# Performance work log

Hardware: AMD Instinct MI355X
Metric: run time of the kernel (lower is better)

Reference implementation:

```python
import jax, jax.numpy as jnp
import numpy as np
import math

D_MODEL = 1024
N_HEADS = 16
D_HEAD = D_MODEL // N_HEADS


def layer_norm(x, gamma, beta, eps=1e-5):
    mu = jnp.mean(x, axis=-1, keepdims=True)
    var = jnp.var(x, axis=-1, keepdims=True)
    return (x - mu) / jnp.sqrt(var + eps) * gamma + beta


def setup_inputs() -> dict:
    key = jax.random.key(0)
    ks = jax.random.split(key, 12)
    B, T, d = 4, 2048, D_MODEL
    s = 0.02
    x = jax.random.normal(ks[0], (B, T, d), dtype=jnp.float32)
    t = jnp.arange(B * T, dtype=jnp.float32).reshape(B, T) % T  # continuous positions
    return {
        "x": x,
        "t": t,
        "w_qkv": jax.random.normal(ks[1], (d, 3 * d), dtype=jnp.float32) * s,
        "b_qkv": jnp.zeros((3 * d,), jnp.float32),
        "w_proj": jax.random.normal(ks[2], (d, d), dtype=jnp.float32) * s,
        "b_proj": jnp.zeros((d,), jnp.float32),
        "g1": jnp.ones((d,), jnp.float32),
        "beta1": jnp.zeros((d,), jnp.float32),
        "g2": jnp.ones((d,), jnp.float32),
        "beta2": jnp.zeros((d,), jnp.float32),
        "w_mlp1": jax.random.normal(ks[3], (d, 4 * d), dtype=jnp.float32) * s,
        "b_mlp1": jnp.zeros((4 * d,), jnp.float32),
        "w_mlp2": jax.random.normal(ks[4], (4 * d, d), dtype=jnp.float32) * s,
        "b_mlp2": jnp.zeros((d,), jnp.float32),
    }


def reference(x, t, w_qkv, b_qkv, w_proj, b_proj, g1, beta1, g2, beta2, w_mlp1, b_mlp1, w_mlp2, b_mlp2):
    B, T, d = x.shape
    H, dh = N_HEADS, D_HEAD
    scale = dh ** -0.5

    h = layer_norm(x, g1, beta1)
    qkv = h @ w_qkv + b_qkv  # [B,T,3d]
    q, k, v = jnp.split(qkv, 3, axis=-1)
    # [B,T,H,dh] -> [B,H,T,dh]
    q = q.reshape(B, T, H, dh).transpose(0, 2, 1, 3)
    k = k.reshape(B, T, H, dh).transpose(0, 2, 1, 3)
    v = v.reshape(B, T, H, dh).transpose(0, 2, 1, 3)

    # ContinuousRoPE on d_head
    half = dh // 2
    freqs = jnp.exp(jnp.arange(half, dtype=jnp.float32) * (-math.log(10000.0) / (half - 1)))
    args = t[:, :, None] * freqs  # [B,T,half]
    cos = jnp.tile(jnp.cos(args), (1, 1, 2))[:, None]  # [B,1,T,dh]
    sin = jnp.tile(jnp.sin(args), (1, 1, 2))[:, None]

    def rotate_half(u):
        u1, u2 = u[..., :dh // 2], u[..., dh // 2:]
        return jnp.concatenate((-u2, u1), axis=-1)

    q = q * cos + rotate_half(q) * sin
    k = k * cos + rotate_half(k) * sin

    attn = jnp.einsum("bhqd,bhkd->bhqk", q, k) * scale  # [B,H,T,T]
    causal = jnp.tril(jnp.ones((T, T), dtype=bool))
    attn = jnp.where(causal, attn, -jnp.inf)
    attn = jax.nn.softmax(attn, axis=-1)
    o = jnp.einsum("bhqk,bhkd->bhqd", attn, v)  # [B,H,T,dh]
    o = o.transpose(0, 2, 1, 3).reshape(B, T, d)

    x1 = o @ w_proj + b_proj + x
    h2 = layer_norm(x1, g2, beta2)
    mlp = jax.nn.gelu(h2 @ w_mlp1 + b_mlp1, approximate=False) @ w_mlp2 + b_mlp2
    return x1 + mlp
```

## Files before the change

### kernel.cpp

```cpp
#include <hip/hip_runtime.h>

typedef __bf16  bf16x8 __attribute__((ext_vector_type(8)));
typedef float   f32x4  __attribute__((ext_vector_type(4)));

typedef const __attribute__((address_space(1))) void* gas_p;
typedef __attribute__((address_space(3))) void*       las_p;

__device__ __forceinline__ void glds16(const void* g, void* l) {
  __builtin_amdgcn_global_load_lds((gas_p)g, (las_p)l, 16, 0, 0);
}

__device__ __forceinline__ ushort f2bf(float f) {
  unsigned u = __float_as_uint(f);
  u += 0x7fffu + ((u >> 16) & 1u);
  return (ushort)(u >> 16);
}

__device__ __forceinline__ void barx() {
  asm volatile("" ::: "memory");
  __builtin_amdgcn_s_barrier();
  asm volatile("" ::: "memory");
}
#define WAITVM(N) asm volatile("s_waitcnt vmcnt(" #N ")" ::: "memory")

__global__ __launch_bounds__(256) void castT_k(const float* __restrict__ w,
                                               ushort* __restrict__ wT,
                                               const int Kd, const int Nd) {
  __shared__ float t[32][33];
  const int nb = blockIdx.x * 32, kb = blockIdx.y * 32;
  const int tx = threadIdx.x & 31, ty = threadIdx.x >> 5;
#pragma unroll
  for (int r = 0; r < 32; r += 8)
    t[ty + r][tx] = w[(size_t)(kb + ty + r) * Nd + nb + tx];
  __syncthreads();
#pragma unroll
  for (int r = 0; r < 32; r += 8)
    wT[(size_t)(nb + ty + r) * Kd + kb + tx] = f2bf(t[tx][ty + r]);
}

__global__ __launch_bounds__(256) void ln_k(const float* __restrict__ x,
                                            const float* __restrict__ gam,
                                            const float* __restrict__ bet,
                                            ushort* __restrict__ out) {
  const int row = blockIdx.x, tid = threadIdx.x;
  const float4 v = ((const float4*)(x + (size_t)row * 1024))[tid];
  float s  = v.x + v.y + v.z + v.w;
  float sq = v.x * v.x + v.y * v.y + v.z * v.z + v.w * v.w;
#pragma unroll
  for (int o = 32; o > 0; o >>= 1) { s += __shfl_xor(s, o); sq += __shfl_xor(sq, o); }
  __shared__ float red[8];
  const int wid = tid >> 6, lane = tid & 63;
  if (lane == 0) { red[wid] = s; red[4 + wid] = sq; }
  __syncthreads();
  s  = red[0] + red[1] + red[2] + red[3];
  sq = red[4] + red[5] + red[6] + red[7];
  const float mu   = s * (1.0f / 1024.0f);
  const float var  = sq * (1.0f / 1024.0f) - mu * mu;
  const float rstd = rsqrtf(var + 1e-5f);
  const float4 gv = ((const float4*)gam)[tid];
  const float4 bv = ((const float4*)bet)[tid];
  ushort4 o4;
  o4.x = f2bf((v.x - mu) * rstd * gv.x + bv.x);
  o4.y = f2bf((v.y - mu) * rstd * gv.y + bv.y);
  o4.z = f2bf((v.z - mu) * rstd * gv.z + bv.z);
  o4.w = f2bf((v.w - mu) * rstd * gv.w + bv.w);
  ((ushort4*)(out + (size_t)row * 1024))[tid] = o4;
}

__global__ __launch_bounds__(256) void vtrans_k(const ushort* __restrict__ Vn,
                                                ushort* __restrict__ Vt) {
  const int bh = blockIdx.y, i0 = blockIdx.x * 64, tid = threadIdx.x;
  __shared__ ushort t[64][65];
  const ushort* src = Vn + (size_t)bh * (2048 * 64);
#pragma unroll
  for (int kk = 0; kk < 16; ++kk) {
    const int e = tid + kk * 256, r = e >> 6, c = e & 63;
    t[r][c] = src[(size_t)(i0 + r) * 64 + c];
  }
  __syncthreads();
  ushort* dst = Vt + (size_t)bh * (64 * 2048);
#pragma unroll
  for (int kk = 0; kk < 16; ++kk) {
    const int e = tid + kk * 256, r = e >> 6, c = e & 63;
    dst[(size_t)r * 2048 + i0 + c] = t[c][r];
  }
}

template <int MF, int EPI>
__global__ __launch_bounds__(512, 2) void gemm2_k(
    const ushort* __restrict__ A, const ushort* __restrict__ Bt,
    const int M, const int N, const int K,
    const float* __restrict__ bias,
    const float* __restrict__ resid,
    float* __restrict__ outf,
    ushort* __restrict__ outb,
    ushort* __restrict__ qo, ushort* __restrict__ ko, ushort* __restrict__ vo) {
  constexpr int BM = MF * 32;
  constexpr int GA = MF / 4;
  extern __shared__ ushort lds_u[];
  ushort* aL = lds_u;
  ushort* bL = lds_u + 4 * BM * 32;

  const int tid = threadIdx.x, wid = tid >> 6, lane = tid & 63;
  const int l15 = lane & 15, g = lane >> 4;
  const int wr = wid >> 2, wc = wid & 3;
  const int m0 = blockIdx.y * BM, n0 = blockIdx.x * 256;

  const int srl = lane >> 2;
  const int scb = ((lane & 3) << 4) ^ (((lane >> 3) & 3) << 4);
  const int rk  = ((l15 >> 1) & 3) << 4;
  const size_t Krow = (size_t)K * 2;

  auto stageA = [&](int b, int kh, int t) {
#pragma unroll
    for (int L = 0; L < GA; ++L) {
      const char* src = (const char*)A + (size_t)(m0 + L * 128 + wid * 16 + srl) * Krow
                        + (size_t)t * 128 + kh * 64 + scb;
      glds16(src, (char*)aL + (size_t)((b * 2 + kh) * BM + L * 128 + wid * 16) * 64);
    }
  };
  auto stageB = [&](int b, int kh, int t) {
#pragma unroll
    for (int L = 0; L < 2; ++L) {
      const char* src = (const char*)Bt + (size_t)(n0 + L * 128 + wid * 16 + srl) * Krow
                        + (size_t)t * 128 + kh * 64 + scb;
      glds16(src, (char*)bL + (size_t)((b * 2 + kh) * 256 + L * 128 + wid * 16) * 64);
    }
  };

  bf16x8 af[MF], bfr[4];
  f32x4 acc[MF][4] = {};

  auto loadA = [&](int b, int kh) {
#pragma unroll
    for (int m = 0; m < MF; ++m)
      af[m] = *(const bf16x8*)((const char*)aL +
          (size_t)((b * 2 + kh) * BM + wr * (BM / 2) + m * 16 + l15) * 64 + ((g * 16) ^ rk));
  };
  auto loadB = [&](int b, int kh, int nh) {
#pragma unroll
    for (int n = 0; n < 2; ++n)
      bfr[nh * 2 + n] = *(const bf16x8*)((const char*)bL +
          (size_t)((b * 2 + kh) * 256 + wc * 64 + (nh * 2 + n) * 16 + l15) * 64 + ((g * 16) ^ rk));
  };
  auto mfma8 = [&](int nh) {
    __builtin_amdgcn_s_setprio(1);
#pragma unroll
    for (int m = 0; m < MF; ++m) {
      acc[m][nh * 2]     = __builtin_amdgcn_mfma_f32_16x16x32_bf16(af[m], bfr[nh * 2],     acc[m][nh * 2],     0, 0, 0);
      acc[m][nh * 2 + 1] = __builtin_amdgcn_mfma_f32_16x16x32_bf16(af[m], bfr[nh * 2 + 1], acc[m][nh * 2 + 1], 0, 0, 0);
    }
    __builtin_amdgcn_s_setprio(0);
  };

  stageA(0, 0, 0); stageB(0, 0, 0); stageA(0, 1, 0); stageB(0, 1, 0);
  if constexpr (MF == 8) { WAITVM(4); } else { WAITVM(3); }
  barx();

  const int nk = K >> 6;
  int cur = 0;
  for (int t = 0; t < nk; ++t) {
    const bool pf = (t + 1 < nk);
    const int nb = cur ^ 1;
    loadA(cur, 0); loadB(cur, 0, 0);
    if (pf) stageA(nb, 0, t + 1);
    barx();
    mfma8(0);
    barx();
    loadB(cur, 0, 1);
    if (pf) stageB(nb, 0, t + 1);
    barx();
    mfma8(1);
    if (pf) { if constexpr (MF == 8) { WAITVM(4); } else { WAITVM(3); } }
    else    { WAITVM(0); }
    barx();
    loadA(cur, 1); loadB(cur, 1, 0);
    if (pf) stageA(nb, 1, t + 1);
    barx();
    mfma8(0);
    barx();
    loadB(cur, 1, 1);
    if (pf) stageB(nb, 1, t + 1);
    barx();
    mfma8(1);
    if (pf) { if constexpr (MF == 8) { WAITVM(4); } else { WAITVM(3); } }
    barx();
    cur = nb;
  }

  const int rb = m0 + wr * (BM / 2);
  const int cb = n0 + wc * 64;
  if constexpr (EPI == 0) {
#pragma unroll
    for (int m = 0; m < MF; ++m)
#pragma unroll
      for (int r = 0; r < 4; ++r) {
        const int s = rb + m * 16 + g * 4 + r;
        const int bb = s >> 11, ii = s & 2047;
#pragma unroll
        for (int n = 0; n < 2; ++n) {
          const int c = cb + n * 16 + l15;
          const int which = c >> 10, h = (c >> 6) & 15, dd = c & 63;
          const float vlo = acc[m][n][r] + bias[c];
          const float vhi = acc[m][n + 2][r] + bias[c + 32];
          const size_t off = ((size_t)((bb * 16 + h) * 2048 + ii)) * 64;
          if (which == 2) {
            vo[off + dd]      = f2bf(vlo);
            vo[off + dd + 32] = f2bf(vhi);
          } else {
            const float fr = __expf(-0.29710776f * (float)dd);
            const float ang = (float)ii * fr;
            const float c0 = cosf(ang), s0 = sinf(ang);
            float rlo = vlo * c0 - vhi * s0;
            float rhi = vhi * c0 + vlo * s0;
            if (which == 0) { rlo *= 0.125f; rhi *= 0.125f; }
            ushort* dst = (which == 0) ? qo : ko;
            dst[off + dd]      = f2bf(rlo);
            dst[off + dd + 32] = f2bf(rhi);
          }
        }
      }
  } else {
#pragma unroll
    for (int m = 0; m < MF; ++m)
#pragma unroll
      for (int n = 0; n < 4; ++n)
#pragma unroll
        for (int r = 0; r < 4; ++r) {
          const int row = rb + m * 16 + g * 4 + r;
          const int col = cb + n * 16 + l15;
          float v = acc[m][n][r] + bias[col];
          if constexpr (EPI == 1) {
            v += resid[(size_t)row * N + col];
            outf[(size_t)row * N + col] = v;
          } else {
            const float ge = 0.5f * v * (1.0f + erff(v * 0.70710678f));
            outb[(size_t)row * N + col] = f2bf(ge);
          }
        }
  }
}

__global__ __launch_bounds__(256) void attn_k(const ushort* __restrict__ Q,
                                              const ushort* __restrict__ K,
                                              const ushort* __restrict__ Vt,
                                              ushort* __restrict__ O) {
  const int bh = blockIdx.x;
  const int qt = 31 - blockIdx.y;
  const int tid = threadIdx.x, wid = tid >> 6, lane = tid & 63;
  const int l15 = lane & 15, g = lane >> 4;
  const size_t bho = (size_t)bh * (2048 * 64);
  const ushort* Qb = Q + bho;
  const char*   KbB = (const char*)(K + bho);
  const char*   VbB = (const char*)(Vt + bho);
  const int b = bh >> 4, h = bh & 15;

  __shared__ ushort kl[2][64 * 64];
  __shared__ ushort vl[2][64 * 64];
  __shared__ ushort pl[4][16 * 64];

  const int rbase = wid * 16;
  const int rsub  = lane >> 3;
  const int cbyte = (lane & 7) << 4;
  const int scb   = cbyte ^ (rsub << 4);

  const int q0 = qt * 64 + wid * 16;

  const bf16x8 qf0 = *(const bf16x8*)&Qb[(size_t)(q0 + l15) * 64 + g * 8];
  const bf16x8 qf1 = *(const bf16x8*)&Qb[(size_t)(q0 + l15) * 64 + 32 + g * 8];

  f32x4 o[4] = {};
  float m = -1e30f, l = 0.f;

  char* pbase = (char*)pl[wid];
  const int swz  = (l15 & 7) << 4;
  const int skey = (l15 & 7) << 4;

  const int nkt = qt + 1;
  {
    const char* ks0 = KbB + (size_t)(0 + rbase + rsub) * 128 + scb;
    const char* vs0 = VbB + (size_t)(rbase + rsub) * 4096 + scb;
    glds16(ks0,            (char*)kl[0] + rbase * 128);
    glds16(ks0 + 8 * 128,  (char*)kl[0] + (rbase + 8) * 128);
    glds16(vs0,            (char*)vl[0] + rbase * 128);
    glds16(vs0 + 8 * 4096, (char*)vl[0] + (rbase + 8) * 128);
  }
  int cur = 0;

  for (int kt = 0; kt < nkt; ++kt) {
    const int k0 = kt * 64;
    __syncthreads();
    if (kt + 1 < nkt) {
      const int nb = cur ^ 1, k1 = k0 + 64;
      const char* ks0 = KbB + (size_t)(k1 + rbase + rsub) * 128 + scb;
      const char* vs0 = VbB + (size_t)(rbase + rsub) * 4096 + (size_t)k1 * 2 + scb;
      glds16(ks0,            (char*)kl[nb] + rbase * 128);
      glds16(ks0 + 8 * 128,  (char*)kl[nb] + (rbase + 8) * 128);
      glds16(vs0,            (char*)vl[nb] + rbase * 128);
      glds16(vs0 + 8 * 4096, (char*)vl[nb] + (rbase + 8) * 128);
    }
    const char* Klds = (const char*)kl[cur];
    const char* Vlds = (const char*)vl[cur];

    f32x4 st[4];
    __builtin_amdgcn_s_setprio(1);
#pragma unroll
    for (int sub = 0; sub < 4; ++sub) {
      const int kr = sub * 16 + l15;
      const bf16x8 kf0 = *(const bf16x8*)(Klds + kr * 128 + ((g * 16) ^ skey));
      const bf16x8 kf1 = *(const bf16x8*)(Klds + kr * 128 + ((64 + g * 16) ^ skey));
      f32x4 z = {0.f, 0.f, 0.f, 0.f};
      f32x4 sv = __builtin_amdgcn_mfma_f32_16x16x32_bf16(kf0, qf0, z, 0, 0, 0);
      sv = __builtin_amdgcn_mfma_f32_16x16x32_bf16(kf1, qf1, sv, 0, 0, 0);
      st[sub] = sv;
    }
    __builtin_amdgcn_s_setprio(0);
    if (k0 + 63 > q0) {
#pragma unroll
      for (int sub = 0; sub < 4; ++sub) {
        const int kk = k0 + sub * 16 + g * 4;
#pragma unroll
        for (int r = 0; r < 4; ++r)
          if (kk + r > q0 + l15) st[sub][r] = -1e30f;
      }
    }
    f32x4 mv = st[0];
#pragma unroll
    for (int sub = 1; sub < 4; ++sub)
#pragma unroll
      for (int r = 0; r < 4; ++r) mv[r] = fmaxf(mv[r], st[sub][r]);
    float tm = fmaxf(fmaxf(mv[0], mv[1]), fmaxf(mv[2], mv[3]));
    tm = fmaxf(tm, __shfl_xor(tm, 16));
    tm = fmaxf(tm, __shfl_xor(tm, 32));
    if (!__all(tm - m <= 8.0f)) {
      const float mnew = fmaxf(m, tm);
      const float corr = __expf(m - mnew);
      m = mnew;
      l *= corr;
      float cr[4];
#pragma unroll
      for (int r = 0; r < 4; ++r) cr[r] = __shfl(corr, g * 4 + r);
#pragma unroll
      for (int nf = 0; nf < 4; ++nf)
#pragma unroll
        for (int r = 0; r < 4; ++r) o[nf][r] *= cr[r];
    }
    float ps = 0.f;
#pragma unroll
    for (int sub = 0; sub < 4; ++sub) {
      const float p0 = __expf(st[sub][0] - m);
      const float p1 = __expf(st[sub][1] - m);
      const float p2 = __expf(st[sub][2] - m);
      const float p3 = __expf(st[sub][3] - m);
      ps += (p0 + p1) + (p2 + p3);
      ushort4 pk;
      pk.x = f2bf(p0); pk.y = f2bf(p1); pk.z = f2bf(p2); pk.w = f2bf(p3);
      *(ushort4*)(pbase + ((l15 * 128 + ((sub * 32 + g * 8) ^ swz)))) = pk;
    }
    ps += __shfl_xor(ps, 16);
    ps += __shfl_xor(ps, 32);
    l += ps;
    const bf16x8 pf0 = *(const bf16x8*)(pbase + (l15 * 128 + ((g * 16) ^ swz)));
    const bf16x8 pf1 = *(const bf16x8*)(pbase + (l15 * 128 + ((64 + g * 16) ^ swz)));
    __builtin_amdgcn_s_setprio(1);
#pragma unroll
    for (int nf = 0; nf < 4; ++nf) {
      const int dr = nf * 16 + l15;
      const bf16x8 vf0 = *(const bf16x8*)(Vlds + dr * 128 + ((g * 16) ^ skey));
      const bf16x8 vf1 = *(const bf16x8*)(Vlds + dr * 128 + ((64 + g * 16) ^ skey));
      o[nf] = __builtin_amdgcn_mfma_f32_16x16x32_bf16(pf0, vf0, o[nf], 0, 0, 0);
      o[nf] = __builtin_amdgcn_mfma_f32_16x16x32_bf16(pf1, vf1, o[nf], 0, 0, 0);
    }
    __builtin_amdgcn_s_setprio(0);
    cur ^= 1;
  }
  const float linv = 1.0f / l;
  float li[4];
#pragma unroll
  for (int r = 0; r < 4; ++r) li[r] = __shfl(linv, g * 4 + r);
#pragma unroll
  for (int nf = 0; nf < 4; ++nf)
#pragma unroll
    for (int r = 0; r < 4; ++r) {
      const int qr = q0 + g * 4 + r;
      O[((size_t)(b * 2048 + qr)) * 1024 + h * 64 + nf * 16 + l15] = f2bf(o[nf][r] * li[r]);
    }
}

extern "C" void kernel_launch(void* const* d_in, const int* in_sizes, int n_in,
                              void* d_out, int out_size, void* d_ws, size_t ws_size,
                              hipStream_t stream) {
  const float* x      = (const float*)d_in[0];
  const float* w_qkv  = (const float*)d_in[2];
  const float* b_qkv  = (const float*)d_in[3];
  const float* w_proj = (const float*)d_in[4];
  const float* b_proj = (const float*)d_in[5];
  const float* g1     = (const float*)d_in[6];
  const float* be1    = (const float*)d_in[7];
  const float* g2     = (const float*)d_in[8];
  const float* be2    = (const float*)d_in[9];
  const float* w_mlp1 = (const float*)d_in[10];
  const float* b_mlp1 = (const float*)d_in[11];
  const float* w_mlp2 = (const float*)d_in[12];
  const float* b_mlp2 = (const float*)d_in[13];

  char* ws = (char*)d_ws;
  ushort* WQKVT  = (ushort*)(ws + 0);
  ushort* WPROJT = (ushort*)(ws + 6291456);
  ushort* WMLP1T = (ushort*)(ws + 8388608);
  ushort* WMLP2T = (ushort*)(ws + 16777216);
  ushort* H      = (ushort*)(ws + 25165824);
  ushort* Qs     = (ushort*)(ws + 41943040);
  ushort* Ks     = (ushort*)(ws + 58720256);
  ushort* Vn     = (ushort*)(ws + 75497472);
  ushort* Vt     = (ushort*)(ws + 92274688);
  ushort* M1     = (ushort*)(ws + 41943040);
  float*  X1     = (float*)(ws + 109051904);

  hipFuncSetAttribute((const void*)gemm2_k<8, 0>, hipFuncAttributeMaxDynamicSharedMemorySize, 131072);
  hipFuncSetAttribute((const void*)gemm2_k<8, 2>, hipFuncAttributeMaxDynamicSharedMemorySize, 131072);
  hipFuncSetAttribute((const void*)gemm2_k<4, 1>, hipFuncAttributeMaxDynamicSharedMemorySize, 98304);

  castT_k<<<dim3(3072 / 32, 1024 / 32), 256, 0, stream>>>(w_qkv, WQKVT, 1024, 3072);
  castT_k<<<dim3(1024 / 32, 1024 / 32), 256, 0, stream>>>(w_proj, WPROJT, 1024, 1024);
  castT_k<<<dim3(4096 / 32, 1024 / 32), 256, 0, stream>>>(w_mlp1, WMLP1T, 1024, 4096);
  castT_k<<<dim3(1024 / 32, 4096 / 32), 256, 0, stream>>>(w_mlp2, WMLP2T, 4096, 1024);

  ln_k<<<8192, 256, 0, stream>>>(x, g1, be1, H);

  gemm2_k<8, 0><<<dim3(3072 / 256, 8192 / 256), 512, 131072, stream>>>(
      H, WQKVT, 8192, 3072, 1024, b_qkv, nullptr, nullptr, nullptr, Qs, Ks, Vn);

  vtrans_k<<<dim3(32, 64), 256, 0, stream>>>(Vn, Vt);

  attn_k<<<dim3(64, 32), 256, 0, stream>>>(Qs, Ks, Vt, H );

  gemm2_k<4, 1><<<dim3(1024 / 256, 8192 / 128), 512, 98304, stream>>>(
      H, WPROJT, 8192, 1024, 1024, b_proj, x, X1, nullptr, nullptr, nullptr, nullptr);

  ln_k<<<8192, 256, 0, stream>>>(X1, g2, be2, H );

  gemm2_k<8, 2><<<dim3(4096 / 256, 8192 / 256), 512, 131072, stream>>>(
      H, WMLP1T, 8192, 4096, 1024, b_mlp1, nullptr, nullptr, M1, nullptr, nullptr, nullptr);

  gemm2_k<4, 1><<<dim3(1024 / 256, 8192 / 128), 512, 98304, stream>>>(
      M1, WMLP2T, 8192, 1024, 4096, b_mlp2, X1, (float*)d_out, nullptr, nullptr, nullptr, nullptr);
}
```

Baseline: 600.4 us.

## Restructure GEMM into triple-buffered K=32 pipeline with tile swizzle and fast erf

Replaces the double-buffered K=64 GEMM main loop, which had many barriers per iteration, with a three-stage ring of K=32 LDS buffers. Loads are issued two steps ahead and each step needs a single barrier. Workgroup indices are remapped in groups of 8 to improve L2 reuse across neighbouring tiles, and the LDS swizzle is adjusted for the 64-byte row width. Exact erff in the GELU epilogue is replaced by an Abramowitz-Stegun polynomial approximation, which is cheaper but adds roughly 1e-7 absolute error before the bf16 rounding.

Result: faster. 568.0 us (-5.4%).

```diff
diff --git a/kernel.cpp b/kernel.cpp
--- a/kernel.cpp
+++ b/kernel.cpp
@@ -22,6 +22,18 @@
   asm volatile("" ::: "memory");
 }
 #define WAITVM(N) asm volatile("s_waitcnt vmcnt(" #N ")" ::: "memory")
+
+__device__ __forceinline__ float erf_fast(float x) {
+  const float ax = fabsf(x);
+  const float t = __frcp_rn(1.0f + 0.3275911f * ax);
+  float p = 1.061405429f;
+  p = p * t - 1.453152027f;
+  p = p * t + 1.421413741f;
+  p = p * t - 0.284496736f;
+  p = p * t + 0.254829592f;
+  const float y = 1.0f - p * t * __expf(-ax * ax);
+  return copysignf(y, x);
+}
 
 __global__ __launch_bounds__(256) void castT_k(const float* __restrict__ w,
                                                ushort* __restrict__ wT,
@@ -87,7 +99,7 @@
 }
 
 template <int MF, int EPI>
-__global__ __launch_bounds__(512, 2) void gemm2_k(
+__global__ __launch_bounds__(512, 2) void gemm3_k(
     const ushort* __restrict__ A, const ushort* __restrict__ Bt,
     const int M, const int N, const int K,
     const float* __restrict__ bias,
@@ -96,96 +108,77 @@
     ushort* __restrict__ outb,
     ushort* __restrict__ qo, ushort* __restrict__ ko, ushort* __restrict__ vo) {
   constexpr int BM = MF * 32;
-  constexpr int GA = MF / 4;
+  constexpr int ACALLS = MF / 4;
   extern __shared__ ushort lds_u[];
   ushort* aL = lds_u;
-  ushort* bL = lds_u + 4 * BM * 32;
+  ushort* bL = lds_u + 3 * BM * 32;
 
   const int tid = threadIdx.x, wid = tid >> 6, lane = tid & 63;
   const int l15 = lane & 15, g = lane >> 4;
   const int wr = wid >> 2, wc = wid & 3;
-  const int m0 = blockIdx.y * BM, n0 = blockIdx.x * 256;
+
+  const int gx = gridDim.x, nwg = gx * gridDim.y;
+  const int f = blockIdx.y * gx + blockIdx.x;
+  const int swz = (f & 7) * (nwg >> 3) + (f >> 3);
+  const int m0 = (swz / gx) * BM, n0 = (swz % gx) * 256;
 
   const int srl = lane >> 2;
-  const int scb = ((lane & 3) << 4) ^ (((lane >> 3) & 3) << 4);
-  const int rk  = ((l15 >> 1) & 3) << 4;
+  const int scb = ((lane & 3) << 4) ^ ((srl & 3) << 4);
+  const int rk  = (l15 & 3) << 4;
   const size_t Krow = (size_t)K * 2;
 
-  auto stageA = [&](int b, int kh, int t) {
-#pragma unroll
-    for (int L = 0; L < GA; ++L) {
-      const char* src = (const char*)A + (size_t)(m0 + L * 128 + wid * 16 + srl) * Krow
-                        + (size_t)t * 128 + kh * 64 + scb;
-      glds16(src, (char*)aL + (size_t)((b * 2 + kh) * BM + L * 128 + wid * 16) * 64);
+  auto stageA = [&](int buf, int t) {
+#pragma unroll
+    for (int L = 0; L < ACALLS; ++L) {
+      const int base = (wid * ACALLS + L) * 16;
+      glds16((const char*)A + (size_t)(m0 + base + srl) * Krow + (size_t)t * 64 + scb,
+             (char*)aL + (size_t)(buf * BM + base) * 64);
     }
   };
-  auto stageB = [&](int b, int kh, int t) {
+  auto stageB = [&](int buf, int t) {
 #pragma unroll
     for (int L = 0; L < 2; ++L) {
-      const char* src = (const char*)Bt + (size_t)(n0 + L * 128 + wid * 16 + srl) * Krow
-                        + (size_t)t * 128 + kh * 64 + scb;
-      glds16(src, (char*)bL + (size_t)((b * 2 + kh) * 256 + L * 128 + wid * 16) * 64);
+      const int base = (wid * 2 + L) * 16;
+      glds16((const char*)Bt + (size_t)(n0 + base + srl) * Krow + (size_t)t * 64 + scb,
+             (char*)bL + (size_t)(buf * 256 + base) * 64);
     }
   };
 
-  bf16x8 af[MF], bfr[4];
   f32x4 acc[MF][4] = {};
 
-  auto loadA = [&](int b, int kh) {
+  stageA(0, 0); stageB(0, 0);
+  stageA(1, 1); stageB(1, 1);
+
+  const int nk = K >> 5;
+  int b0 = 0;
+  for (int t = 0; t < nk; ++t) {
+    if (t + 2 < nk) {
+      if constexpr (MF == 8) { WAITVM(4); } else { WAITVM(3); }
+    } else {
+      WAITVM(0);
+    }
+    barx();
+    if (t + 2 < nk) {
+      int nbuf = b0 + 2; if (nbuf >= 3) nbuf -= 3;
+      stageA(nbuf, t + 2); stageB(nbuf, t + 2);
+    }
+    bf16x8 af[MF], bfr[4];
 #pragma unroll
     for (int m = 0; m < MF; ++m)
       af[m] = *(const bf16x8*)((const char*)aL +
-          (size_t)((b * 2 + kh) * BM + wr * (BM / 2) + m * 16 + l15) * 64 + ((g * 16) ^ rk));
-  };
-  auto loadB = [&](int b, int kh, int nh) {
-#pragma unroll
-    for (int n = 0; n < 2; ++n)
-      bfr[nh * 2 + n] = *(const bf16x8*)((const char*)bL +
-          (size_t)((b * 2 + kh) * 256 + wc * 64 + (nh * 2 + n) * 16 + l15) * 64 + ((g * 16) ^ rk));
-  };
-  auto mfma8 = [&](int nh) {
+          (size_t)(b0 * BM + wr * (BM / 2) + m * 16 + l15) * 64 + ((g * 16) ^ rk));
+#pragma unroll
+    for (int n = 0; n < 4; ++n)
+      bfr[n] = *(const bf16x8*)((const char*)bL +
+          (size_t)(b0 * 256 + wc * 64 + n * 16 + l15) * 64 + ((g * 16) ^ rk));
     __builtin_amdgcn_s_setprio(1);
 #pragma unroll
-    for (int m = 0; m < MF; ++m) {
-      acc[m][nh * 2]     = __builtin_amdgcn_mfma_f32_16x16x32_bf16(af[m], bfr[nh * 2],     acc[m][nh * 2],     0, 0, 0);
-      acc[m][nh * 2 + 1] = __builtin_amdgcn_mfma_f32_16x16x32_bf16(af[m], bfr[nh * 2 + 1], acc[m][nh * 2 + 1], 0, 0, 0);
-    }
+    for (int m = 0; m < MF; ++m)
+#pragma unroll
+      for (int n = 0; n < 4; ++n)
+        acc[m][n] = __builtin_amdgcn_mfma_f32_16x16x32_bf16(af[m], bfr[n], acc[m][n], 0, 0, 0);
     __builtin_amdgcn_s_setprio(0);
-  };
-
-  stageA(0, 0, 0); stageB(0, 0, 0); stageA(0, 1, 0); stageB(0, 1, 0);
-  if constexpr (MF == 8) { WAITVM(4); } else { WAITVM(3); }
-  barx();
-
-  const int nk = K >> 6;
-  int cur = 0;
-  for (int t = 0; t < nk; ++t) {
-    const bool pf = (t + 1 < nk);
-    const int nb = cur ^ 1;
-    loadA(cur, 0); loadB(cur, 0, 0);
-    if (pf) stageA(nb, 0, t + 1);
-    barx();
-    mfma8(0);
-    barx();
-    loadB(cur, 0, 1);
-    if (pf) stageB(nb, 0, t + 1);
-    barx();
-    mfma8(1);
-    if (pf) { if constexpr (MF == 8) { WAITVM(4); } else { WAITVM(3); } }
-    else    { WAITVM(0); }
-    barx();
-    loadA(cur, 1); loadB(cur, 1, 0);
-    if (pf) stageA(nb, 1, t + 1);
-    barx();
-    mfma8(0);
-    barx();
-    loadB(cur, 1, 1);
-    if (pf) stageB(nb, 1, t + 1);
-    barx();
-    mfma8(1);
-    if (pf) { if constexpr (MF == 8) { WAITVM(4); } else { WAITVM(3); } }
-    barx();
-    cur = nb;
+    ++b0; if (b0 == 3) b0 = 0;
   }
 
   const int rb = m0 + wr * (BM / 2);
@@ -234,7 +227,7 @@
             v += resid[(size_t)row * N + col];
             outf[(size_t)row * N + col] = v;
           } else {
-            const float ge = 0.5f * v * (1.0f + erff(v * 0.70710678f));
+            const float ge = 0.5f * v * (1.0f + erf_fast(v * 0.70710678f));
             outb[(size_t)row * N + col] = f2bf(ge);
           }
         }
@@ -417,9 +410,9 @@
   ushort* M1     = (ushort*)(ws + 41943040);
   float*  X1     = (float*)(ws + 109051904);
 
-  hipFuncSetAttribute((const void*)gemm2_k<8, 0>, hipFuncAttributeMaxDynamicSharedMemorySize, 131072);
-  hipFuncSetAttribute((const void*)gemm2_k<8, 2>, hipFuncAttributeMaxDynamicSharedMemorySize, 131072);
-  hipFuncSetAttribute((const void*)gemm2_k<4, 1>, hipFuncAttributeMaxDynamicSharedMemorySize, 98304);
+  hipFuncSetAttribute((const void*)gemm3_k<8, 0>, hipFuncAttributeMaxDynamicSharedMemorySize, 98304);
+  hipFuncSetAttribute((const void*)gemm3_k<8, 2>, hipFuncAttributeMaxDynamicSharedMemorySize, 98304);
+  hipFuncSetAttribute((const void*)gemm3_k<4, 1>, hipFuncAttributeMaxDynamicSharedMemorySize, 73728);
 
   castT_k<<<dim3(3072 / 32, 1024 / 32), 256, 0, stream>>>(w_qkv, WQKVT, 1024, 3072);
   castT_k<<<dim3(1024 / 32, 1024 / 32), 256, 0, stream>>>(w_proj, WPROJT, 1024, 1024);
@@ -428,21 +421,21 @@
 
   ln_k<<<8192, 256, 0, stream>>>(x, g1, be1, H);
 
-  gemm2_k<8, 0><<<dim3(3072 / 256, 8192 / 256), 512, 131072, stream>>>(
+  gemm3_k<8, 0><<<dim3(3072 / 256, 8192 / 256), 512, 98304, stream>>>(
       H, WQKVT, 8192, 3072, 1024, b_qkv, nullptr, nullptr, nullptr, Qs, Ks, Vn);
 
   vtrans_k<<<dim3(32, 64), 256, 0, stream>>>(Vn, Vt);
 
   attn_k<<<dim3(64, 32), 256, 0, stream>>>(Qs, Ks, Vt, H );
 
-  gemm2_k<4, 1><<<dim3(1024 / 256, 8192 / 128), 512, 98304, stream>>>(
+  gemm3_k<4, 1><<<dim3(1024 / 256, 8192 / 128), 512, 73728, stream>>>(
       H, WPROJT, 8192, 1024, 1024, b_proj, x, X1, nullptr, nullptr, nullptr, nullptr);
 
   ln_k<<<8192, 256, 0, stream>>>(X1, g2, be2, H );
 
-  gemm2_k<8, 2><<<dim3(4096 / 256, 8192 / 256), 512, 131072, stream>>>(
+  gemm3_k<8, 2><<<dim3(4096 / 256, 8192 / 256), 512, 98304, stream>>>(
       H, WMLP1T, 8192, 4096, 1024, b_mlp1, nullptr, nullptr, M1, nullptr, nullptr, nullptr);
 
-  gemm2_k<4, 1><<<dim3(1024 / 256, 8192 / 128), 512, 98304, stream>>>(
+  gemm3_k<4, 1><<<dim3(1024 / 256, 8192 / 128), 512, 73728, stream>>>(
       M1, WMLP2T, 8192, 1024, 4096, b_mlp2, X1, (float*)d_out, nullptr, nullptr, nullptr, nullptr);
 }
```
